# Kernel optimization log

Measured on AMD Instinct MI355X. Metric: run time of the kernel, lower is better.

## Reference

```python
import jax, jax.numpy as jnp
import numpy as np

B, T, D, N, K, H = 2, 2048, 2048, 16, 8, 128
WINDOW = 1024
SOFT_CAP = 50.0
Q_SCALE = H ** -0.5  # query_pre_attn_scalar
ROPE_BASE = 10000
ROPE_SCALE = 1.0
K_MASK = -2.3819763e38


def apply_rope(x, positions, base_frequency=ROPE_BASE, scale_factor=ROPE_SCALE):
    # x: [B, T, n, H], positions: [B, T]
    head_dim = x.shape[-1]
    fraction = 2.0 * jnp.arange(head_dim // 2, dtype=jnp.float32) / head_dim
    timescale = base_frequency ** fraction  # [H/2]
    sin_inp = positions[..., None].astype(jnp.float32) / timescale  # [B,T,H/2]
    sin_inp = sin_inp[..., None, :] / scale_factor  # [B,T,1,H/2]
    sin, cos = jnp.sin(sin_inp), jnp.cos(sin_inp)
    x1, x2 = jnp.split(x, 2, axis=-1)
    out = jnp.concatenate([x1 * cos - x2 * sin, x2 * cos + x1 * sin], axis=-1)
    return out.astype(x.dtype)


def rms_norm(x, scale, eps=1e-6):
    var = jnp.mean(jnp.square(x.astype(jnp.float32)), axis=-1, keepdims=True)
    normed = x * jax.lax.rsqrt(var + eps)
    return (normed * (1.0 + scale)).astype(x.dtype)


def setup_inputs() -> dict:
    key = jax.random.key(0)
    ks = jax.random.split(key, 4)
    x = jax.random.normal(ks[0], (B, T, D), jnp.float32)
    segment_pos = jnp.tile(jnp.arange(T, dtype=jnp.int32)[None, :], (B, 1))
    attn_mask = jnp.tril(jnp.ones((T, T), dtype=bool))[None].repeat(B, axis=0)
    w_q = jax.random.normal(ks[1], (N, D, H), jnp.float32) * (D ** -0.5)
    w_kv = jax.random.normal(ks[2], (2, K, D, H), jnp.float32) * (D ** -0.5)
    w_o = jax.random.normal(ks[3], (N, H, D), jnp.float32) * ((N * H) ** -0.5)
    q_norm_scale = jnp.zeros((H,), jnp.float32)
    k_norm_scale = jnp.zeros((H,), jnp.float32)
    return dict(x=x, w_q=w_q, w_kv=w_kv, w_o=w_o,
                q_norm_scale=q_norm_scale, k_norm_scale=k_norm_scale,
                segment_pos=segment_pos, attn_mask=attn_mask)


def reference(x, w_q, w_kv, w_o, q_norm_scale, k_norm_scale, segment_pos, attn_mask):
    # projections
    q = jnp.einsum('BTD,NDH->BTNH', x, w_q)              # [B,T,N,H]
    kv = jnp.einsum('BSD,CKDH->CBSKH', x, w_kv)          # [2,B,S,K,H]
    k, v = kv[0], kv[1]
    # QK RMSNorm
    q = rms_norm(q, q_norm_scale)
    k = rms_norm(k, k_norm_scale)
    # RoPE + query scaling
    q = apply_rope(q, segment_pos) * Q_SCALE
    k = apply_rope(k, segment_pos)
    # GQA logits
    G = N // K
    qg = q.reshape(B, T, K, G, H)
    logits = jnp.einsum('BTKGH,BSKH->BTKGS', qg, k).reshape(B, T, N, T)
    # soft cap
    logits = jnp.tanh(logits / SOFT_CAP) * SOFT_CAP
    # sliding-window mask combined with causal attn_mask
    pos_q = segment_pos[:, :, None]
    pos_k = segment_pos[:, None, :]
    sliding = (pos_k > pos_q - WINDOW) & (pos_k < pos_q + WINDOW)
    mask = attn_mask & sliding                           # [B,T,S]
    padded = jnp.where(mask[:, :, None, :], logits, K_MASK)
    probs = jax.nn.softmax(padded, axis=-1).astype(k.dtype)
    # GQA weighted values
    enc = jnp.einsum('BTKGS,BSKH->BTKGH', probs.reshape(B, T, K, G, T), v)
    enc = enc.reshape(B, T, N, H)
    # split/concat of navigator vs scribe heads is an identity on output
    return jnp.einsum('BTNH,NHD->BTD', enc, w_o)
```

## Files before the change

### kernel.cpp

```cpp
#include <hip/hip_runtime.h>
#include <hip/hip_bf16.h>
#include <stdint.h>

typedef __attribute__((ext_vector_type(8))) short short8;
typedef __attribute__((ext_vector_type(4))) float f32x4;

#define B_ 2
#define T_ 2048
#define D_ 2048
#define N_ 16
#define KH_ 8
#define H_ 128
#define WINDOW_ 1024

__device__ __forceinline__ uint16_t f2bf(float f) {
  union { float f; uint32_t u; } a; a.f = f;
  uint32_t u = a.u;
  return (uint16_t)((u + 0x7FFFu + ((u >> 16) & 1u)) >> 16);
}
__device__ __forceinline__ float bf2f(uint16_t u) {
  union { uint32_t u; float f; } a; a.u = (uint32_t)u << 16;
  return a.f;
}

__device__ __forceinline__ void gl_lds16(const void* g, void* l) {
  __builtin_amdgcn_global_load_lds((const __attribute__((address_space(1))) void*)g,
                                   (__attribute__((address_space(3))) void*)l, 16, 0, 0);
}

__global__ __launch_bounds__(256) void k_f2b4(const float* __restrict__ src,
                                              uint16_t* __restrict__ dst, long n) {
  long i = ((long)blockIdx.x * 256 + threadIdx.x) * 4;
  if (i >= n) return;
  float4 v = *(const float4*)(src + i);
  uint64_t p = (uint64_t)f2bf(v.x) | ((uint64_t)f2bf(v.y) << 16) |
               ((uint64_t)f2bf(v.z) << 32) | ((uint64_t)f2bf(v.w) << 48);
  *(uint64_t*)(dst + i) = p;
}

__global__ __launch_bounds__(256)
void k_prep_qkv(const float* __restrict__ w_q, const float* __restrict__ w_kv,
                uint16_t* __restrict__ wq_t, uint16_t* __restrict__ wkv_t) {
  __shared__ float tile[32][33];
  int z = blockIdx.z;
  const float* s;
  uint16_t* d;
  if (z < 16) {
    s = w_q + (long)z * D_ * H_;
    d = wq_t + (long)z * H_ * D_;
  } else if (z < 24) {
    s = w_kv + (long)(z - 16) * D_ * H_;
    d = wkv_t + (long)(z - 16) * H_ * D_;
  } else {
    s = w_kv + (long)KH_ * D_ * H_ + (long)(z - 24) * D_ * H_;
    d = wkv_t + (long)1024 * 2048 + (long)(z - 24) * H_ * D_;
  }
  int c0 = blockIdx.x * 32, r0 = blockIdx.y * 32;
  int x = threadIdx.x, y = threadIdx.y;
#pragma unroll
  for (int j = 0; j < 4; ++j)
    tile[y + j * 8][x] = s[(long)(r0 + y + j * 8) * H_ + (c0 + x)];
  __syncthreads();
#pragma unroll
  for (int j = 0; j < 4; ++j)
    d[(long)(c0 + y + j * 8) * D_ + (r0 + x)] = f2bf(tile[x][y + j * 8]);
}

__global__ __launch_bounds__(256)
void k_transpose_f2b(const float* __restrict__ src, uint16_t* __restrict__ dst,
                     int R, int C, int nb1, long sbs1, long sbs2, long dbs,
                     long src_off, int srs) {
  __shared__ float tile[32][33];
  int z = blockIdx.z;
  int b1 = z % nb1, b2 = z / nb1;
  const float* s = src + src_off + (long)b1 * sbs1 + (long)b2 * sbs2;
  uint16_t* d = dst + (long)z * dbs;
  int c0 = blockIdx.x * 32, r0 = blockIdx.y * 32;
  int x = threadIdx.x, y = threadIdx.y;
#pragma unroll
  for (int j = 0; j < 4; ++j)
    tile[y + j * 8][x] = s[(long)(r0 + y + j * 8) * srs + (c0 + x)];
  __syncthreads();
#pragma unroll
  for (int j = 0; j < 4; ++j)
    d[(long)(c0 + y + j * 8) * R + (r0 + x)] = f2bf(tile[x][y + j * 8]);
}

__global__ __launch_bounds__(256)
void k_transpose_v(const uint16_t* __restrict__ kvg, uint16_t* __restrict__ vbt) {
  __shared__ uint16_t tile[32][33];
  int z = blockIdx.z;
  int kh = z % KH_, b = z / KH_;
  const uint16_t* s = kvg + (long)b * T_ * 2048 + 1024 + kh * H_;
  uint16_t* d = vbt + (long)z * H_ * T_;
  int h0 = blockIdx.x * 32, s0 = blockIdx.y * 32;
  int x = threadIdx.x, y = threadIdx.y;
#pragma unroll
  for (int j = 0; j < 4; ++j)
    tile[y + j * 8][x] = s[(long)(s0 + y + j * 8) * 2048 + (h0 + x)];
  __syncthreads();
#pragma unroll
  for (int j = 0; j < 4; ++j) {
    int h = h0 + y + j * 8;
    int si = s0 + x;
    int ss = (si & ~63) | ((((si >> 3) & 7) ^ (h & 7)) << 3) | (si & 7);
    d[(long)h * T_ + ss] = tile[x][y + j * 8];
  }
}

__global__ __launch_bounds__(512, 2)
void k_gemm8(const uint16_t* __restrict__ A, const uint16_t* __restrict__ Bt,
             uint16_t* __restrict__ C0, uint16_t* __restrict__ C1, int nbx, int splitc) {
  __shared__ __align__(16) uint16_t Ls[2][2][2][128 * 64];
  int tid = threadIdx.x, lane = tid & 63, w = tid >> 6;
  int wm = w >> 2, wn = w & 3;
  int fr = lane & 15, fgrp = lane >> 4;
  int bid = blockIdx.x;
  int k2 = bid >> 3;
  long by = (bid & 7) * 2 + k2 / nbx;
  long bx = k2 % nbx;
  long row0 = by * 256, col0 = bx * 256;

  int trow = tid >> 3;
  int kse = (((tid & 7) * 16) ^ ((trow & 7) << 4)) >> 1;
  const uint16_t* aS[2] = { A + (row0 + trow) * 2048 + kse,
                            A + (row0 + 128 + trow) * 2048 + kse };
  const uint16_t* bS[2] = { Bt + (col0 + trow) * 2048 + kse,
                            Bt + (col0 + 128 + trow) * 2048 + kse };
  char* ldsbase = (char*)Ls + w * 1024;

  int kx[2] = { (fgrp * 16) ^ ((fr & 7) << 4), (64 + fgrp * 16) ^ ((fr & 7) << 4) };
  int aoffb = (wm * 64 + fr) * 128;
  int boffb = (wn * 32 + fr) * 128;
  const char* LA = (const char*)Ls;
  const char* LB = LA + 65536;

  f32x4 acc[2][2][4][2];
#pragma unroll
  for (int qm = 0; qm < 2; ++qm)
#pragma unroll
    for (int qn = 0; qn < 2; ++qn)
#pragma unroll
      for (int m = 0; m < 4; ++m)
#pragma unroll
        for (int n = 0; n < 2; ++n) acc[qm][qn][m][n] = (f32x4){0.f, 0.f, 0.f, 0.f};

  short8 RA[4][2];
  short8 RB[2][2][2];

#define STG(MAT, SLOT, HALF, KT) do {                                      \
    const uint16_t* _g = (MAT ? bS[HALF] : aS[HALF]) + (KT) * 64;          \
    char* _l = ldsbase + (MAT) * 65536 + (SLOT) * 32768 + (HALF) * 16384;  \
    gl_lds16(_g, _l);                                                      \
    gl_lds16(_g + 64 * 2048, _l + 8192);                                   \
  } while (0)

#define RDA(SLOT, QM) do {                                                             \
    _Pragma("unroll") for (int m = 0; m < 4; ++m) {                                    \
      RA[m][0] = *(const short8*)(LA + (SLOT)*32768 + (QM)*16384 + aoffb + m*2048 + kx[0]); \
      RA[m][1] = *(const short8*)(LA + (SLOT)*32768 + (QM)*16384 + aoffb + m*2048 + kx[1]); } \
  } while (0)

#define RDB(SLOT, QN) do {                                                             \
    _Pragma("unroll") for (int n = 0; n < 2; ++n) {                                    \
      RB[QN][n][0] = *(const short8*)(LB + (SLOT)*32768 + (QN)*16384 + boffb + n*2048 + kx[0]); \
      RB[QN][n][1] = *(const short8*)(LB + (SLOT)*32768 + (QN)*16384 + boffb + n*2048 + kx[1]); } \
  } while (0)

#define PHX(RDSTMT, STGSTMT, QM, QN, VM) do {                                         \
    RDSTMT;                                                                           \
    STGSTMT;                                                                          \
    __builtin_amdgcn_s_barrier();                                                     \
    asm volatile("s_waitcnt lgkmcnt(0)" ::: "memory");                                \
    __builtin_amdgcn_sched_barrier(0);                                                \
    __builtin_amdgcn_s_setprio(1);                                                    \
    _Pragma("unroll") for (int m = 0; m < 4; ++m)                                     \
      _Pragma("unroll") for (int n = 0; n < 2; ++n) {                                 \
        acc[QM][QN][m][n] = __builtin_amdgcn_mfma_f32_16x16x32_bf16(RA[m][0], RB[QN][n][0], acc[QM][QN][m][n], 0, 0, 0); \
        acc[QM][QN][m][n] = __builtin_amdgcn_mfma_f32_16x16x32_bf16(RA[m][1], RB[QN][n][1], acc[QM][QN][m][n], 0, 0, 0); } \
    __builtin_amdgcn_s_setprio(0);                                                    \
    if (VM) { asm volatile("s_waitcnt vmcnt(8)" ::: "memory");                        \
              __builtin_amdgcn_sched_barrier(0); }                                    \
    __builtin_amdgcn_s_barrier();                                                     \
    __builtin_amdgcn_sched_barrier(0);                                                \
  } while (0)

  STG(0, 0, 0, 0); STG(1, 0, 0, 0); STG(1, 0, 1, 0); STG(0, 0, 1, 0);
  STG(0, 1, 0, 1); STG(1, 1, 0, 1); STG(1, 1, 1, 1); STG(0, 1, 1, 1);
  asm volatile("s_waitcnt vmcnt(8)" ::: "memory");
  __builtin_amdgcn_sched_barrier(0);
  __builtin_amdgcn_s_barrier();

#pragma unroll 1
  for (int it = 0; it < 16; ++it) {
    int t2 = (2 * it + 2) & 31, t3 = (2 * it + 3) & 31;
    PHX({ RDA(0, 0); RDB(0, 0); }, {}, 0, 0, 0);
    PHX({ RDB(0, 1); }, { STG(0, 0, 0, t2); STG(1, 0, 0, t2); }, 0, 1, 0);
    PHX({ RDA(0, 1); }, { STG(1, 0, 1, t2); }, 1, 1, 0);
    PHX({}, { STG(0, 0, 1, t2); }, 1, 0, 1);
    PHX({ RDA(1, 0); RDB(1, 0); }, {}, 0, 0, 0);
    PHX({ RDB(1, 1); }, { STG(0, 1, 0, t3); STG(1, 1, 0, t3); }, 0, 1, 0);
    PHX({ RDA(1, 1); }, { STG(1, 1, 1, t3); }, 1, 1, 0);
    PHX({}, { STG(0, 1, 1, t3); }, 1, 0, 1);
  }
#undef PHX
#undef RDA
#undef RDB
#undef STG

  int og = fgrp * 4;
  bool hic = (col0 >= splitc);
  uint16_t* Cb = hic ? C1 : C0;
  long cb = col0 - (hic ? splitc : 0);
#pragma unroll
  for (int qm = 0; qm < 2; ++qm)
#pragma unroll
    for (int qn = 0; qn < 2; ++qn)
#pragma unroll
      for (int m = 0; m < 4; ++m)
#pragma unroll
        for (int n = 0; n < 2; ++n) {
          long r = row0 + qm * 128 + wm * 64 + m * 16 + og;
          long c = cb + qn * 128 + wn * 32 + n * 16 + fr;
          uint16_t* cp = Cb + r * 2048 + c;
#pragma unroll
          for (int i = 0; i < 4; ++i) cp[(long)i * 2048] = f2bf(acc[qm][qn][m][n][i]);
        }
}

__global__ __launch_bounds__(512, 2)
void k_gemm8n(const uint16_t* __restrict__ A, const uint16_t* __restrict__ Bt,
              float* __restrict__ C, int nbx) {
  __shared__ __align__(16) uint16_t LsA[2][2][128 * 64];
  __shared__ __align__(16) uint16_t LsB[2][128 * 64];
  int tid = threadIdx.x, lane = tid & 63, w = tid >> 6;
  int wm = w >> 2, wn = w & 3;
  int fr = lane & 15, fgrp = lane >> 4;
  int bid = blockIdx.x;
  int k2 = bid >> 3;
  long by = (bid & 7) * 2 + k2 / nbx;
  long bx = k2 % nbx;
  long row0 = by * 256, col0 = bx * 128;

  int trow = tid >> 3;
  int kse = (((tid & 7) * 16) ^ ((trow & 7) << 4)) >> 1;
  const uint16_t* aS[2] = { A + (row0 + trow) * 2048 + kse,
                            A + (row0 + 128 + trow) * 2048 + kse };
  const uint16_t* bS = Bt + (col0 + trow) * 2048 + kse;
  char* ldsA_w = (char*)LsA + w * 1024;
  char* ldsB_w = (char*)LsB + w * 1024;

  int kx[2] = { (fgrp * 16) ^ ((fr & 7) << 4), (64 + fgrp * 16) ^ ((fr & 7) << 4) };
  int aoffb = (wm * 64 + fr) * 128;
  int boffb = (wn * 32 + fr) * 128;
  const char* LA = (const char*)LsA;
  const char* LB = (const char*)LsB;

  f32x4 acc[2][4][2];
#pragma unroll
  for (int qm = 0; qm < 2; ++qm)
#pragma unroll
    for (int m = 0; m < 4; ++m)
#pragma unroll
      for (int n = 0; n < 2; ++n) acc[qm][m][n] = (f32x4){0.f, 0.f, 0.f, 0.f};

#define STGA(SLOT, HALF, KT) do {                                \
    const uint16_t* _g = aS[HALF] + (KT) * 64;                   \
    char* _l = ldsA_w + (SLOT) * 32768 + (HALF) * 16384;         \
    gl_lds16(_g, _l);                                            \
    gl_lds16(_g + 64 * 2048, _l + 8192);                         \
  } while (0)
#define STGB(SLOT, KT) do {                                      \
    const uint16_t* _g = bS + (KT) * 64;                         \
    char* _l = ldsB_w + (SLOT) * 16384;                          \
    gl_lds16(_g, _l);                                            \
    gl_lds16(_g + 64 * 2048, _l + 8192);                         \
  } while (0)

#define PHN(SLOT, QM, STMT, VM) do {                                                  \
    short8 _a[4][2], _b[2][2];                                                        \
    _Pragma("unroll") for (int m = 0; m < 4; ++m) {                                   \
      _a[m][0] = *(const short8*)(LA + (SLOT)*32768 + (QM)*16384 + aoffb + m*2048 + kx[0]); \
      _a[m][1] = *(const short8*)(LA + (SLOT)*32768 + (QM)*16384 + aoffb + m*2048 + kx[1]); } \
    _Pragma("unroll") for (int n = 0; n < 2; ++n) {                                   \
      _b[n][0] = *(const short8*)(LB + (SLOT)*16384 + boffb + n*2048 + kx[0]);        \
      _b[n][1] = *(const short8*)(LB + (SLOT)*16384 + boffb + n*2048 + kx[1]); }      \
    STMT;                                                                             \
    __builtin_amdgcn_s_barrier();                                                     \
    asm volatile("s_waitcnt lgkmcnt(0)" ::: "memory");                                \
    __builtin_amdgcn_sched_barrier(0);                                                \
    __builtin_amdgcn_s_setprio(1);                                                    \
    _Pragma("unroll") for (int m = 0; m < 4; ++m)                                     \
      _Pragma("unroll") for (int n = 0; n < 2; ++n) {                                 \
        acc[QM][m][n] = __builtin_amdgcn_mfma_f32_16x16x32_bf16(_a[m][0], _b[n][0], acc[QM][m][n], 0, 0, 0); \
        acc[QM][m][n] = __builtin_amdgcn_mfma_f32_16x16x32_bf16(_a[m][1], _b[n][1], acc[QM][m][n], 0, 0, 0); } \
    __builtin_amdgcn_s_setprio(0);                                                    \
    if (VM) { asm volatile("s_waitcnt vmcnt(2)" ::: "memory");                        \
              __builtin_amdgcn_sched_barrier(0); }                                    \
    __builtin_amdgcn_s_barrier();                                                     \
    __builtin_amdgcn_sched_barrier(0);                                                \
  } while (0)

  STGA(0, 0, 0); STGA(0, 1, 0); STGB(0, 0); STGA(1, 0, 1);
  asm volatile("s_waitcnt vmcnt(2)" ::: "memory");
  __builtin_amdgcn_sched_barrier(0);
  __builtin_amdgcn_s_barrier();

#pragma unroll 1
  for (int it = 0; it < 16; ++it) {
    int t1 = 2 * it + 1, t2 = (2 * it + 2) & 31, t3 = (2 * it + 3) & 31;
    PHN(0, 0, { STGA(1, 1, t1); STGB(1, t1); }, 0);
    PHN(0, 1, STGA(0, 0, t2), 1);
    PHN(1, 0, { STGA(0, 1, t2); STGB(0, t2); }, 0);
    PHN(1, 1, STGA(1, 0, t3), 1);
  }
#undef PHN
#undef STGA
#undef STGB

  int og = fgrp * 4;
#pragma unroll
  for (int qm = 0; qm < 2; ++qm)
#pragma unroll
    for (int m = 0; m < 4; ++m)
#pragma unroll
      for (int n = 0; n < 2; ++n) {
        long r = row0 + qm * 128 + wm * 64 + m * 16 + og;
        long c = col0 + wn * 32 + n * 16 + fr;
        float* cp = C + r * 2048 + c;
#pragma unroll
        for (int i = 0; i < 4; ++i) cp[(long)i * 2048] = acc[qm][m][n][i];
      }
}

__global__ __launch_bounds__(256)
void k_qpost(const uint16_t* __restrict__ qg, const float* __restrict__ qs,
             uint16_t* __restrict__ qb) {
  int gw = blockIdx.x * 4 + (threadIdx.x >> 6);
  int lane = threadIdx.x & 63;
  int bt = gw / N_;
  int t = bt % T_;
  const uint16_t* src = qg + (long)gw * H_;
  float x1 = bf2f(src[lane]), x2 = bf2f(src[lane + 64]);
  float ssq = x1 * x1 + x2 * x2;
#pragma unroll
  for (int off = 1; off < 64; off <<= 1) ssq += __shfl_xor(ssq, off);
  float inv = rsqrtf(ssq * (1.0f / 128.0f) + 1e-6f);
  float n1 = x1 * inv * (1.0f + qs[lane]);
  float n2 = x2 * inv * (1.0f + qs[lane + 64]);
  float ts = powf(10000.0f, (float)lane * (2.0f / 128.0f));
  float ang = (float)t / ts;
  float sn, cs;
  sincosf(ang, &sn, &cs);
  const float QSC = 0.08838834764831845f;
  uint16_t* dp = qb + (long)gw * H_;
  dp[lane] = f2bf((n1 * cs - n2 * sn) * QSC);
  dp[lane + 64] = f2bf((n2 * cs + n1 * sn) * QSC);
}

__global__ __launch_bounds__(256)
void k_kpost(const uint16_t* __restrict__ kvg, const float* __restrict__ ks,
             uint16_t* __restrict__ kb) {
  int gw = blockIdx.x * 4 + (threadIdx.x >> 6);
  int lane = threadIdx.x & 63;
  int kh = gw % KH_;
  int bt = gw / KH_;
  int t = bt % T_, b = bt / T_;
  const uint16_t* src = kvg + (long)bt * (KH_ * H_ * 2) + kh * H_;
  float x1 = bf2f(src[lane]), x2 = bf2f(src[lane + 64]);
  float ssq = x1 * x1 + x2 * x2;
#pragma unroll
  for (int off = 1; off < 64; off <<= 1) ssq += __shfl_xor(ssq, off);
  float inv = rsqrtf(ssq * (1.0f / 128.0f) + 1e-6f);
  float n1 = x1 * inv * (1.0f + ks[lane]);
  float n2 = x2 * inv * (1.0f + ks[lane + 64]);
  float ts = powf(10000.0f, (float)lane * (2.0f / 128.0f));
  float ang = (float)t / ts;
  float sn, cs;
  sincosf(ang, &sn, &cs);
  int sw = (t & 7) << 3;
  uint16_t* dp = kb + ((long)(b * KH_ + kh) * T_ + t) * H_;
  dp[lane ^ sw] = f2bf(n1 * cs - n2 * sn);
  dp[(lane + 64) ^ sw] = f2bf(n2 * cs + n1 * sn);
}

__global__ __launch_bounds__(256, 4)
void k_attn(const uint16_t* __restrict__ qb, const uint16_t* __restrict__ kb,
            const uint16_t* __restrict__ vbt, uint16_t* __restrict__ enc) {
  __shared__ uint16_t Ks[64 * 128];
  __shared__ uint16_t Vs[128 * 64];
  __shared__ uint16_t Pl[4][16 * 64];
  int tid = threadIdx.x, lane = tid & 63, w = tid >> 6;
  int nt = T_ / 64;
  int blk = blockIdx.x;
  int tq = nt - 1 - (blk >> 5);
  int bn = blk & 31;
  int n = bn % N_, b = bn / N_;
  int kh = n >> 1;
  int t0 = tq * 64;
  int tw = t0 + w * 16;
  int fr = lane & 15, fgrp = lane >> 4, fk = fgrp * 8;
  int sw3 = fr & 7;

  const uint16_t* qrow = qb + ((long)(b * T_ + tw + fr) * N_ + n) * H_;
  short8 aq[4];
#pragma unroll
  for (int kk = 0; kk < 4; ++kk) aq[kk] = *(const short8*)(qrow + kk * 32 + fk);

  float lrow[4];
  f32x4 o[8];
#pragma unroll
  for (int i = 0; i < 4; ++i) lrow[i] = 0.0f;
#pragma unroll
  for (int hf = 0; hf < 8; ++hf) o[hf] = (f32x4){0.f, 0.f, 0.f, 0.f};

  int s_begin = t0 - (WINDOW_ - 1);
  if (s_begin < 0) s_begin = 0;
  s_begin &= ~63;
  int s_endex = t0 + 64;

  const uint16_t* kbase = kb + (long)(b * KH_ + kh) * T_ * H_;
  const uint16_t* vbase = vbt + (long)(b * KH_ + kh) * H_ * T_;
  int krow_st = tid >> 4, kcol_st = (tid & 15) * 8;
  int vrow_st = tid >> 3, vcol_st = (tid & 7) * 8;
  char* ldsK = (char*)Ks + w * 1024;
  char* ldsV = (char*)Vs + w * 1024;
  uint16_t* Pw = Pl[w];

  for (int s0 = s_begin; s0 < s_endex; s0 += 64) {
    __syncthreads();
#pragma unroll
    for (int j = 0; j < 4; ++j) {
      gl_lds16(kbase + (long)(s0 + j * 16 + krow_st) * H_ + kcol_st, ldsK + j * 4096);
      gl_lds16(vbase + (long)(j * 32 + vrow_st) * T_ + s0 + vcol_st, ldsV + j * 4096);
    }
    __syncthreads();
    if (s0 > tw + 15 || s0 + 63 < tw - (WINDOW_ - 1)) continue;

    f32x4 sc[4];
#pragma unroll
    for (int kc = 0; kc < 4; ++kc) {
      f32x4 a = (f32x4){0.f, 0.f, 0.f, 0.f};
      const uint16_t* kr = Ks + (kc * 16 + fr) * 128;
#pragma unroll
      for (int kk = 0; kk < 4; ++kk) {
        short8 bk = *(const short8*)(kr + ((((kk << 2) | fgrp) ^ sw3) << 3));
        a = __builtin_amdgcn_mfma_f32_16x16x32_bf16(aq[kk], bk, a, 0, 0, 0);
      }
      sc[kc] = a;
    }

    bool full = (s0 + 63 <= tw) && (s0 >= tw + 16 - WINDOW_);
#define SMBODY(FULL)                                                              \
    _Pragma("unroll") for (int i = 0; i < 4; ++i) {                               \
      int r = fgrp * 4 + i;                                                       \
      int rsw = (r & 7) << 3;                                                     \
      int trowq = tw + r;                                                         \
      float ps = 0.f;                                                             \
      _Pragma("unroll") for (int kc = 0; kc < 4; ++kc) {                          \
        float v = sc[kc][i];                                                      \
        float u = v * v * 4.0e-4f;                                                \
        float t50 = v * fmaf(u, fmaf(u, fmaf(u, -0.053968254f, 0.13333334f),      \
                                     -0.33333334f), 1.0f);                        \
        float p = __expf(t50 - 20.0f);                                            \
        if (!(FULL)) {                                                            \
          int s = s0 + kc * 16 + fr;                                              \
          bool ok = (s <= trowq) && (s > trowq - WINDOW_);                        \
          p = ok ? p : 0.0f;                                                      \
        }                                                                         \
        ps += p;                                                                  \
        *(__hip_bfloat16*)(Pw + r * 64 + ((kc * 16 + fr) ^ rsw)) =                \
            __float2bfloat16(p);                                                  \
      }                                                                           \
      lrow[i] += ps;                                                              \
    }
    if (full) { SMBODY(true) } else { SMBODY(false) }
#undef SMBODY

    short8 pa0 = *(const short8*)(Pw + fr * 64 + ((fgrp ^ sw3) << 3));
    short8 pa1 = *(const short8*)(Pw + fr * 64 + (((4 | fgrp) ^ sw3) << 3));
#pragma unroll
    for (int hf = 0; hf < 8; ++hf) {
      const uint16_t* vr = Vs + (hf * 16 + fr) * 64;
      short8 bv0 = *(const short8*)(vr + ((fgrp ^ sw3) << 3));
      short8 bv1 = *(const short8*)(vr + (((4 | fgrp) ^ sw3) << 3));
      o[hf] = __builtin_amdgcn_mfma_f32_16x16x32_bf16(pa0, bv0, o[hf], 0, 0, 0);
      o[hf] = __builtin_amdgcn_mfma_f32_16x16x32_bf16(pa1, bv1, o[hf], 0, 0, 0);
    }
  }

#pragma unroll
  for (int i = 0; i < 4; ++i) {
#pragma unroll
    for (int off = 1; off < 16; off <<= 1) lrow[i] += __shfl_xor(lrow[i], off);
    lrow[i] = 1.0f / lrow[i];
  }
#pragma unroll
  for (int hf = 0; hf < 8; ++hf)
#pragma unroll
    for (int i = 0; i < 4; ++i) {
      int t = tw + fgrp * 4 + i;
      float val = o[hf][i] * lrow[i];
      enc[((long)(b * T_ + t) * N_ + n) * H_ + hf * 16 + fr] = f2bf(val);
    }
}

extern "C" void kernel_launch(void* const* d_in, const int* in_sizes, int n_in,
                              void* d_out, int out_size, void* d_ws, size_t ws_size,
                              hipStream_t stream) {
  const float* x = (const float*)d_in[0];
  const float* w_q = (const float*)d_in[1];
  const float* w_kv = (const float*)d_in[2];
  const float* w_o = (const float*)d_in[3];
  const float* qns = (const float*)d_in[4];
  const float* kns = (const float*)d_in[5];
  float* out = (float*)d_out;

  uint16_t* ws = (uint16_t*)d_ws;
  uint16_t* xb    = ws;
  uint16_t* wq_t  = xb    + 8388608;
  uint16_t* wkv_t = wq_t  + 4194304;
  uint16_t* wo_t  = wkv_t + 4194304;
  uint16_t* qb    = wo_t  + 4194304;
  uint16_t* kb    = qb    + 8388608;
  uint16_t* vbt   = kb    + 4194304;
  uint16_t* enc   = vbt   + 4194304;
  uint16_t* qg_b  = enc   + 8388608;
  uint16_t* kvg_b = qg_b  + 8388608;
  if (ws_size < (size_t)125829120) return;

  dim3 tb(32, 8);
  k_f2b4<<<8192, 256, 0, stream>>>(x, xb, 8388608);
  k_prep_qkv<<<dim3(4, 64, 32), tb, 0, stream>>>(w_q, w_kv, wq_t, wkv_t);
  k_transpose_f2b<<<dim3(64, 64, 1), tb, 0, stream>>>(w_o, wo_t, 2048, 2048, 1,
      0, 0, 0, 0, 2048);
  k_gemm8<<<256, 512, 0, stream>>>(xb, wq_t, qg_b, kvg_b, 16, 2048);
  k_qpost<<<(B_ * T_ * N_) / 4, 256, 0, stream>>>(qg_b, qns, qb);
  k_kpost<<<(B_ * T_ * KH_) / 4, 256, 0, stream>>>(kvg_b, kns, kb);
  k_transpose_v<<<dim3(4, 64, 16), tb, 0, stream>>>(kvg_b, vbt);
  k_attn<<<B_ * N_ * (T_ / 64), 256, 0, stream>>>(qb, kb, vbt, enc);
  k_gemm8n<<<256, 512, 0, stream>>>(enc, wo_t, out, 16);
}
```

Baseline: 223.7 us.

## Double-buffer K/V LDS tiles in attention kernel to overlap loads with compute

```diff
diff --git a/kernel.cpp b/kernel.cpp
--- a/kernel.cpp
+++ b/kernel.cpp
@@ -384,11 +384,11 @@
   dp[(lane + 64) ^ sw] = f2bf(n2 * cs + n1 * sn);
 }
 
-__global__ __launch_bounds__(256, 4)
+__global__ __launch_bounds__(256, 2)
 void k_attn(const uint16_t* __restrict__ qb, const uint16_t* __restrict__ kb,
             const uint16_t* __restrict__ vbt, uint16_t* __restrict__ enc) {
-  __shared__ uint16_t Ks[64 * 128];
-  __shared__ uint16_t Vs[128 * 64];
+  __shared__ uint16_t Ks[2][64 * 128];
+  __shared__ uint16_t Vs[2][128 * 64];
   __shared__ uint16_t Pl[4][16 * 64];
   int tid = threadIdx.x, lane = tid & 63, w = tid >> 6;
   int nt = T_ / 64;
@@ -418,76 +418,89 @@
   if (s_begin < 0) s_begin = 0;
   s_begin &= ~63;
   int s_endex = t0 + 64;
+  int nloc = (s_endex - s_begin) >> 6;
 
   const uint16_t* kbase = kb + (long)(b * KH_ + kh) * T_ * H_;
   const uint16_t* vbase = vbt + (long)(b * KH_ + kh) * H_ * T_;
   int krow_st = tid >> 4, kcol_st = (tid & 15) * 8;
   int vrow_st = tid >> 3, vcol_st = (tid & 7) * 8;
-  char* ldsK = (char*)Ks + w * 1024;
-  char* ldsV = (char*)Vs + w * 1024;
   uint16_t* Pw = Pl[w];
 
-  for (int s0 = s_begin; s0 < s_endex; s0 += 64) {
-    __syncthreads();
-#pragma unroll
-    for (int j = 0; j < 4; ++j) {
-      gl_lds16(kbase + (long)(s0 + j * 16 + krow_st) * H_ + kcol_st, ldsK + j * 4096);
-      gl_lds16(vbase + (long)(j * 32 + vrow_st) * T_ + s0 + vcol_st, ldsV + j * 4096);
+#define STAGEKV(BUF, S0) do {                                                        \
+    char* _lk = (char*)Ks + (BUF) * 16384 + w * 1024;                                \
+    char* _lv = (char*)Vs + (BUF) * 16384 + w * 1024;                                \
+    _Pragma("unroll") for (int j = 0; j < 4; ++j) {                                  \
+      gl_lds16(kbase + (long)((S0) + j * 16 + krow_st) * H_ + kcol_st, _lk + j * 4096); \
+      gl_lds16(vbase + (long)(j * 32 + vrow_st) * T_ + (S0) + vcol_st, _lv + j * 4096); \
+    }                                                                                \
+  } while (0)
+
+  STAGEKV(0, s_begin);
+  __syncthreads();
+
+  for (int it = 0; it < nloc; ++it) {
+    int s0 = s_begin + (it << 6);
+    int cur = it & 1;
+    if (it + 1 < nloc) STAGEKV(cur ^ 1, s0 + 64);
+
+    if (!(s0 > tw + 15 || s0 + 63 < tw - (WINDOW_ - 1))) {
+      const uint16_t* Kc = (const uint16_t*)Ks + cur * 8192;
+      const uint16_t* Vc = (const uint16_t*)Vs + cur * 8192;
+
+      f32x4 sc[4];
+#pragma unroll
+      for (int kc = 0; kc < 4; ++kc) {
+        f32x4 a = (f32x4){0.f, 0.f, 0.f, 0.f};
+        const uint16_t* kr = Kc + (kc * 16 + fr) * 128;
+#pragma unroll
+        for (int kk = 0; kk < 4; ++kk) {
+          short8 bk = *(const short8*)(kr + ((((kk << 2) | fgrp) ^ sw3) << 3));
+          a = __builtin_amdgcn_mfma_f32_16x16x32_bf16(aq[kk], bk, a, 0, 0, 0);
+        }
+        sc[kc] = a;
+      }
+
+      bool full = (s0 + 63 <= tw) && (s0 >= tw + 16 - WINDOW_);
+#define SMBODY(FULL)                                                              \
+      _Pragma("unroll") for (int i = 0; i < 4; ++i) {                             \
+        int r = fgrp * 4 + i;                                                     \
+        int rsw = (r & 7) << 3;                                                   \
+        int trowq = tw + r;                                                       \
+        float ps = 0.f;                                                           \
+        _Pragma("unroll") for (int kc = 0; kc < 4; ++kc) {                        \
+          float v = sc[kc][i];                                                    \
+          float u = v * v * 4.0e-4f;                                              \
+          float t50 = v * fmaf(u, fmaf(u, fmaf(u, -0.053968254f, 0.13333334f),    \
+                                       -0.33333334f), 1.0f);                      \
+          float p = __expf(t50 - 20.0f);                                          \
+          if (!(FULL)) {                                                          \
+            int s = s0 + kc * 16 + fr;                                            \
+            bool ok = (s <= trowq) && (s > trowq - WINDOW_);                      \
+            p = ok ? p : 0.0f;                                                    \
+          }                                                                       \
+          ps += p;                                                                \
+          *(__hip_bfloat16*)(Pw + r * 64 + ((kc * 16 + fr) ^ rsw)) =              \
+              __float2bfloat16(p);                                                \
+        }                                                                         \
+        lrow[i] += ps;                                                            \
+      }
+      if (full) { SMBODY(true) } else { SMBODY(false) }
+#undef SMBODY
+
+      short8 pa0 = *(const short8*)(Pw + fr * 64 + ((fgrp ^ sw3) << 3));
+      short8 pa1 = *(const short8*)(Pw + fr * 64 + (((4 | fgrp) ^ sw3) << 3));
+#pragma unroll
+      for (int hf = 0; hf < 8; ++hf) {
+        const uint16_t* vr = Vc + (hf * 16 + fr) * 64;
+        short8 bv0 = *(const short8*)(vr + ((fgrp ^ sw3) << 3));
+        short8 bv1 = *(const short8*)(vr + (((4 | fgrp) ^ sw3) << 3));
+        o[hf] = __builtin_amdgcn_mfma_f32_16x16x32_bf16(pa0, bv0, o[hf], 0, 0, 0);
+        o[hf] = __builtin_amdgcn_mfma_f32_16x16x32_bf16(pa1, bv1, o[hf], 0, 0, 0);
+      }
     }
     __syncthreads();
-    if (s0 > tw + 15 || s0 + 63 < tw - (WINDOW_ - 1)) continue;
-
-    f32x4 sc[4];
-#pragma unroll
-    for (int kc = 0; kc < 4; ++kc) {
-      f32x4 a = (f32x4){0.f, 0.f, 0.f, 0.f};
-      const uint16_t* kr = Ks + (kc * 16 + fr) * 128;
-#pragma unroll
-      for (int kk = 0; kk < 4; ++kk) {
-        short8 bk = *(const short8*)(kr + ((((kk << 2) | fgrp) ^ sw3) << 3));
-        a = __builtin_amdgcn_mfma_f32_16x16x32_bf16(aq[kk], bk, a, 0, 0, 0);
-      }
-      sc[kc] = a;
-    }
-
-    bool full = (s0 + 63 <= tw) && (s0 >= tw + 16 - WINDOW_);
-#define SMBODY(FULL)                                                              \
-    _Pragma("unroll") for (int i = 0; i < 4; ++i) {                               \
-      int r = fgrp * 4 + i;                                                       \
-      int rsw = (r & 7) << 3;                                                     \
-      int trowq = tw + r;                                                         \
-      float ps = 0.f;                                                             \
-      _Pragma("unroll") for (int kc = 0; kc < 4; ++kc) {                          \
-        float v = sc[kc][i];                                                      \
-        float u = v * v * 4.0e-4f;                                                \
-        float t50 = v * fmaf(u, fmaf(u, fmaf(u, -0.053968254f, 0.13333334f),      \
-                                     -0.33333334f), 1.0f);                        \
-        float p = __expf(t50 - 20.0f);                                            \
-        if (!(FULL)) {                                                            \
-          int s = s0 + kc * 16 + fr;                                              \
-          bool ok = (s <= trowq) && (s > trowq - WINDOW_);                        \
-          p = ok ? p : 0.0f;                                                      \
-        }                                                                         \
-        ps += p;                                                                  \
-        *(__hip_bfloat16*)(Pw + r * 64 + ((kc * 16 + fr) ^ rsw)) =                \
-            __float2bfloat16(p);                                                  \
-      }                                                                           \
-      lrow[i] += ps;                                                              \
-    }
-    if (full) { SMBODY(true) } else { SMBODY(false) }
-#undef SMBODY
-
-    short8 pa0 = *(const short8*)(Pw + fr * 64 + ((fgrp ^ sw3) << 3));
-    short8 pa1 = *(const short8*)(Pw + fr * 64 + (((4 | fgrp) ^ sw3) << 3));
-#pragma unroll
-    for (int hf = 0; hf < 8; ++hf) {
-      const uint16_t* vr = Vs + (hf * 16 + fr) * 64;
-      short8 bv0 = *(const short8*)(vr + ((fgrp ^ sw3) << 3));
-      short8 bv1 = *(const short8*)(vr + (((4 | fgrp) ^ sw3) << 3));
-      o[hf] = __builtin_amdgcn_mfma_f32_16x16x32_bf16(pa0, bv0, o[hf], 0, 0, 0);
-      o[hf] = __builtin_amdgcn_mfma_f32_16x16x32_bf16(pa1, bv1, o[hf], 0, 0, 0);
-    }
   }
+#undef STAGEKV
 
 #pragma unroll
   for (int i = 0; i < 4; ++i) {
```

Measured after the change: 228.1 us. No clear change (+2.0%).
